# Kernel tuning notes

Measured on AMD Instinct MI355X. Metric: run time of the kernel, lower is better.

Reference implementation:

```python
import jax, jax.numpy as jnp
import numpy as np

HIDDEN = 1024
HEADS = 16
D_HEAD = HIDDEN // HEADS  # 64
N = 2048


def setup_inputs() -> dict:
    key = jax.random.key(0)
    ks = jax.random.split(key, 12)
    s = 1.0 / np.sqrt(HIDDEN)
    return {
        "q": jax.random.normal(ks[0], (N, HIDDEN), jnp.float32),
        "k": jax.random.normal(ks[1], (N, HIDDEN), jnp.float32),
        "v": jax.random.normal(ks[2], (N, HIDDEN), jnp.float32),
        "attn_bias": jax.random.normal(ks[3], (HEADS, 1, N, N), jnp.float32),
        "Wq": jax.random.normal(ks[4], (HIDDEN, HIDDEN), jnp.float32) * s,
        "bq": jax.random.normal(ks[5], (HIDDEN,), jnp.float32) * s,
        "Wk": jax.random.normal(ks[6], (HIDDEN, HIDDEN), jnp.float32) * s,
        "bk": jax.random.normal(ks[7], (HIDDEN,), jnp.float32) * s,
        "Wv": jax.random.normal(ks[8], (HIDDEN, HIDDEN), jnp.float32) * s,
        "bv": jax.random.normal(ks[9], (HIDDEN,), jnp.float32) * s,
        "Wo": jax.random.normal(ks[10], (HIDDEN, HIDDEN), jnp.float32) * s,
        "bo": jax.random.normal(ks[11], (HIDDEN,), jnp.float32) * s,
    }


def reference(q, k, v, attn_bias, Wq, bq, Wk, bk, Wv, bv, Wo, bo):
    # q,k,v: [N, hidden]; attn_bias: [H, 1, N, N]. Attention runs over the
    # node axis (dim 0 in the torch code), inner seq dim is 1 (squeezed).
    n = q.shape[0]
    scale = D_HEAD ** -0.5
    qh = (q @ Wq.T + bq).reshape(n, HEADS, D_HEAD).transpose(1, 0, 2)  # [H,N,d]
    kh = (k @ Wk.T + bk).reshape(n, HEADS, D_HEAD).transpose(1, 0, 2)  # [H,N,d]
    vh = (v @ Wv.T + bv).reshape(n, HEADS, D_HEAD).transpose(1, 0, 2)  # [H,N,d]
    scores = jnp.einsum('hnd,hmd->hnm', qh * scale, kh) + attn_bias[:, 0]  # [H,N,N]
    attn = jax.nn.softmax(scores, axis=-1)
    ctx = jnp.einsum('hnm,hmd->hnd', attn, vh)            # [H,N,d]
    ctx = ctx.transpose(1, 0, 2).reshape(n, HEADS * D_HEAD)  # [N,hidden]
    return ctx @ Wo.T + bo
```

## Files before the change

### kernel.cpp

```cpp
#include <hip/hip_runtime.h>
#include <type_traits>
#include <utility>

#define NT 2048
#define HD 1024
#define NHEAD 16
#define DHEAD 64
#define LOG2E 1.44269504f

typedef float f32x4 __attribute__((ext_vector_type(4)));
typedef __bf16 b16x8 __attribute__((ext_vector_type(8)));
typedef short s16x8 __attribute__((ext_vector_type(8)));
typedef unsigned short u16x8 __attribute__((ext_vector_type(8)));
typedef unsigned short u16x4 __attribute__((ext_vector_type(4)));

template <typename V, typename = void>
struct mfma_takes : std::false_type {};
template <typename V>
struct mfma_takes<V, std::void_t<decltype(__builtin_amdgcn_mfma_f32_16x16x32_bf16(
                         std::declval<V>(), std::declval<V>(), std::declval<f32x4>(), 0, 0, 0))>>
    : std::true_type {};

template <typename V>
__device__ __forceinline__ f32x4 mfma_impl(V a, V b, f32x4 c) {
  return __builtin_amdgcn_mfma_f32_16x16x32_bf16(a, b, c, 0, 0, 0);
}

__device__ __forceinline__ f32x4 mfma_bf16(u16x8 a, u16x8 b, f32x4 c) {
  using V = typename std::conditional<mfma_takes<b16x8>::value, b16x8, s16x8>::type;
  return mfma_impl<V>(__builtin_bit_cast(V, a), __builtin_bit_cast(V, b), c);
}

__device__ __forceinline__ unsigned short f2bf(float f) {
  unsigned int u = __builtin_bit_cast(unsigned int, f);
  return (unsigned short)((u + 0x7FFFu + ((u >> 16) & 1u)) >> 16);
}

__device__ __forceinline__ void gload16(const unsigned short* g, unsigned short* l) {
  __builtin_amdgcn_global_load_lds(
      (__attribute__((address_space(1))) void*)(void*)(g),
      (__attribute__((address_space(3))) void*)(void*)(l), 16, 0, 0);
}

__global__ __launch_bounds__(256) void cvt_bf16(
    const float* __restrict__ s0, const float* __restrict__ s1, const float* __restrict__ s2,
    const float* __restrict__ s3, const float* __restrict__ s4, const float* __restrict__ s5,
    const float* __restrict__ s6,
    unsigned short* __restrict__ d0, unsigned short* __restrict__ d1, unsigned short* __restrict__ d2,
    unsigned short* __restrict__ d3, unsigned short* __restrict__ d4, unsigned short* __restrict__ d5,
    unsigned short* __restrict__ d6) {
  const int seg = blockIdx.y;
  const float* s;
  unsigned short* d;
  switch (seg) {
    case 0: s = s0; d = d0; break;
    case 1: s = s1; d = d1; break;
    case 2: s = s2; d = d2; break;
    case 3: s = s3; d = d3; break;
    case 4: s = s4; d = d4; break;
    case 5: s = s5; d = d5; break;
    default: s = s6; d = d6; break;
  }
  const int n = (seg < 3) ? NT * HD : HD * HD;
  for (int i = blockIdx.x * 2048 + threadIdx.x * 8; i < n; i += gridDim.x * 2048) {
    f32x4 f0 = *reinterpret_cast<const f32x4*>(&s[i]);
    f32x4 f1 = *reinterpret_cast<const f32x4*>(&s[i + 4]);
    u16x8 o;
#pragma unroll
    for (int e = 0; e < 4; ++e) { o[e] = f2bf(f0[e]); o[e + 4] = f2bf(f1[e]); }
    *reinterpret_cast<u16x8*>(&d[i]) = o;
  }
}

__device__ __forceinline__ void gemm64x128(
    const unsigned short* __restrict__ A, const unsigned short* __restrict__ B,
    int n0, int m0,
    unsigned short* As0, unsigned short* As1,
    unsigned short* Bs0, unsigned short* Bs1, f32x4 acc[2][4]) {
  const int tid = threadIdx.x;
  const int lane = tid & 63;
  const int wr = (tid >> 6) >> 1, wc = (tid >> 6) & 1;
  const int srow = tid >> 3;
  const int scol = (tid & 7) << 3;

  auto stage = [&](int kt, unsigned short* as, unsigned short* bs) {
#pragma unroll
    for (int p = 0; p < 2; ++p)
      gload16(&A[(size_t)(n0 + p * 32 + srow) * HD + kt + scol], as + p * 2048 + tid * 8);
#pragma unroll
    for (int p = 0; p < 4; ++p)
      gload16(&B[(size_t)(m0 + p * 32 + srow) * HD + kt + scol], bs + p * 2048 + tid * 8);
  };
  auto comp = [&](const unsigned short* as, const unsigned short* bs) {
#pragma unroll
    for (int ks = 0; ks < 2; ++ks) {
      const int kcol = ks * 32 + (lane >> 4) * 8;
      u16x8 a[2], b[4];
#pragma unroll
      for (int i = 0; i < 2; ++i)
        a[i] = *reinterpret_cast<const u16x8*>(&as[(wr * 32 + i * 16 + (lane & 15)) * 64 + kcol]);
#pragma unroll
      for (int j = 0; j < 4; ++j)
        b[j] = *reinterpret_cast<const u16x8*>(&bs[(wc * 64 + j * 16 + (lane & 15)) * 64 + kcol]);
#pragma unroll
      for (int i = 0; i < 2; ++i)
#pragma unroll
        for (int j = 0; j < 4; ++j)
          acc[i][j] = mfma_bf16(a[i], b[j], acc[i][j]);
    }
  };

  stage(0, As0, Bs0);
  __syncthreads();
#pragma unroll 1
  for (int tt = 0; tt < 8; ++tt) {
    const int kt = tt * 128;
    stage(kt + 64, As1, Bs1);
    comp(As0, Bs0);
    __syncthreads();
    if (kt + 128 < HD) stage(kt + 128, As0, Bs0);
    comp(As1, Bs1);
    __syncthreads();
  }
}

__global__ __launch_bounds__(256) void proj_gemm(
    const unsigned short* __restrict__ qb, const unsigned short* __restrict__ kb,
    const unsigned short* __restrict__ vb,
    const unsigned short* __restrict__ Wqb, const unsigned short* __restrict__ Wkb,
    const unsigned short* __restrict__ Wvb,
    const float* __restrict__ bq, const float* __restrict__ bk, const float* __restrict__ bv,
    unsigned short* __restrict__ Qh, unsigned short* __restrict__ Kh,
    unsigned short* __restrict__ Vt) {
  const int L = blockIdx.x;
  const int m = L / 96;
  const int c = L % 96;
  const int z = c / 32;
  const int n = c % 32;
  const int n0 = n * 64, m0 = m * 128;

  const unsigned short* A = (z == 0) ? qb : (z == 1) ? kb : vb;
  const unsigned short* B = (z == 0) ? Wqb : (z == 1) ? Wkb : Wvb;
  const float* bias = (z == 0) ? bq : (z == 1) ? bk : bv;

  __shared__ unsigned short As0[64 * 64], As1[64 * 64];
  __shared__ unsigned short Bs0[128 * 64], Bs1[128 * 64];

  const int tid = threadIdx.x;
  const int lane = tid & 63;
  const int wr = (tid >> 6) >> 1, wc = (tid >> 6) & 1;

  f32x4 acc[2][4] = {};
  gemm64x128(A, B, n0, m0, As0, As1, Bs0, Bs1, acc);

  const int rgrp = (lane >> 4) * 4;
  const float scale = (z == 0) ? 0.125f * LOG2E : 1.0f;
#pragma unroll
  for (int i = 0; i < 2; ++i) {
    const int nb = n0 + wr * 32 + i * 16 + rgrp;
#pragma unroll
    for (int j = 0; j < 4; ++j) {
      const int mcol = m0 + wc * 64 + j * 16 + (lane & 15);
      const float bb = bias[mcol];
      if (z == 2) {
        u16x4 pk;
#pragma unroll
        for (int r = 0; r < 4; ++r) pk[r] = f2bf(acc[i][j][r] + bb);
        *reinterpret_cast<u16x4*>(&Vt[(size_t)mcol * NT + nb]) = pk;
      } else {
        unsigned short* dst = (z == 0) ? Qh : Kh;
#pragma unroll
        for (int r = 0; r < 4; ++r)
          dst[(size_t)(nb + r) * HD + mcol] = f2bf((acc[i][j][r] + bb) * scale);
      }
    }
  }
}

__global__ __launch_bounds__(256) void attn_kernel(
    const unsigned short* __restrict__ Qh, const unsigned short* __restrict__ Kh,
    const unsigned short* __restrict__ Vt, const float* __restrict__ bias,
    unsigned short* __restrict__ ctx) {
  const int id = blockIdx.x;
  const int xcd = id & 7, slot = id >> 3;
  const int h = xcd * 2 + (slot >> 5);
  const int q0 = (slot & 31) * 64;
  const int tid = threadIdx.x;
  const int lane = tid & 63;
  const int wave = tid >> 6;

  __shared__ unsigned short Ks[128][72];
  __shared__ unsigned short Vs[64][136];
  __shared__ unsigned short Ps[4][16][136];

  u16x8 qf[2];
  {
    const int qrow = q0 + wave * 16 + (lane & 15);
    const int db = (lane >> 4) * 8;
    qf[0] = *reinterpret_cast<const u16x8*>(&Qh[(size_t)qrow * HD + h * DHEAD + db]);
    qf[1] = *reinterpret_cast<const u16x8*>(&Qh[(size_t)qrow * HD + h * DHEAD + 32 + db]);
  }

  f32x4 oacc[4] = {};
  float mrun[4], lrun[4];
#pragma unroll
  for (int r = 0; r < 4; ++r) { mrun[r] = -3.0e38f; lrun[r] = 0.f; }

  const float* bias_h = bias + (size_t)h * NT * NT;
  const int qlrow = q0 + wave * 16 + (lane >> 4) * 4;

  const int ksr = tid >> 3, ksc = (tid & 7) << 3;
  const int vsd = tid >> 2, vsc = (tid & 3) << 3;
  const unsigned short* Kbase = Kh + h * DHEAD;
  const unsigned short* Vbase = Vt + (size_t)(h * DHEAD + vsd) * NT;

#pragma unroll
  for (int p = 0; p < 4; ++p)
    *reinterpret_cast<u16x8*>(&Ks[ksr + p * 32][ksc]) =
        *reinterpret_cast<const u16x8*>(&Kbase[(size_t)(ksr + p * 32) * HD + ksc]);
#pragma unroll
  for (int p = 0; p < 4; ++p)
    *reinterpret_cast<u16x8*>(&Vs[vsd][vsc + p * 32]) =
        *reinterpret_cast<const u16x8*>(&Vbase[vsc + p * 32]);
  __syncthreads();

  for (int t = 0; t < NT / 128; ++t) {
    const int kt = t * 128;
    float br[8][4];
    const float* bp = bias_h + (size_t)qlrow * NT + kt + (lane & 15);
#pragma unroll
    for (int j = 0; j < 8; ++j)
#pragma unroll
      for (int r = 0; r < 4; ++r) br[j][r] = bp[(size_t)r * NT + j * 16];

    u16x8 kpre[4], vpre[4];
    const bool more = (t + 1 < NT / 128);
    if (more) {
      const int kt2 = kt + 128;
#pragma unroll
      for (int p = 0; p < 4; ++p)
        kpre[p] = *reinterpret_cast<const u16x8*>(&Kbase[(size_t)(kt2 + ksr + p * 32) * HD + ksc]);
#pragma unroll
      for (int p = 0; p < 4; ++p)
        vpre[p] = *reinterpret_cast<const u16x8*>(&Vbase[kt2 + vsc + p * 32]);
    }

    f32x4 s[8] = {};
#pragma unroll
    for (int ks = 0; ks < 2; ++ks) {
      const int kcol = ks * 32 + (lane >> 4) * 8;
#pragma unroll
      for (int j = 0; j < 8; ++j) {
        u16x8 kf = *reinterpret_cast<const u16x8*>(&Ks[j * 16 + (lane & 15)][kcol]);
        s[j] = mfma_bf16(qf[ks], kf, s[j]);
      }
    }
#pragma unroll
    for (int j = 0; j < 8; ++j)
#pragma unroll
      for (int r = 0; r < 4; ++r) s[j][r] = fmaf(br[j][r], LOG2E, s[j][r]);

    float mnew[4];
#pragma unroll
    for (int r = 0; r < 4; ++r) {
      float mx = s[0][r];
#pragma unroll
      for (int j = 1; j < 8; ++j) mx = fmaxf(mx, s[j][r]);
      mx = fmaxf(mx, __shfl_xor(mx, 1));
      mx = fmaxf(mx, __shfl_xor(mx, 2));
      mx = fmaxf(mx, __shfl_xor(mx, 4));
      mx = fmaxf(mx, __shfl_xor(mx, 8));
      mnew[r] = fmaxf(mrun[r], mx);
    }
#pragma unroll
    for (int r = 0; r < 4; ++r) {
      const float corr = exp2f(mrun[r] - mnew[r]);
      lrun[r] *= corr;
#pragma unroll
      for (int nd = 0; nd < 4; ++nd) oacc[nd][r] *= corr;
      mrun[r] = mnew[r];
    }
    float psum[4] = {0.f, 0.f, 0.f, 0.f};
#pragma unroll
    for (int j = 0; j < 8; ++j)
#pragma unroll
      for (int r = 0; r < 4; ++r) {
        const float p = exp2f(s[j][r] - mrun[r]);
        psum[r] += p;
        Ps[wave][(lane >> 4) * 4 + r][j * 16 + (lane & 15)] = f2bf(p);
      }
#pragma unroll
    for (int r = 0; r < 4; ++r) {
      float tsum = psum[r];
      tsum += __shfl_xor(tsum, 1);
      tsum += __shfl_xor(tsum, 2);
      tsum += __shfl_xor(tsum, 4);
      tsum += __shfl_xor(tsum, 8);
      lrun[r] += tsum;
    }

#pragma unroll
    for (int kk = 0; kk < 4; ++kk) {
      const int kcol = kk * 32 + (lane >> 4) * 8;
      u16x8 pa = *reinterpret_cast<const u16x8*>(&Ps[wave][lane & 15][kcol]);
#pragma unroll
      for (int nd = 0; nd < 4; ++nd) {
        u16x8 vb = *reinterpret_cast<const u16x8*>(&Vs[nd * 16 + (lane & 15)][kcol]);
        oacc[nd] = mfma_bf16(pa, vb, oacc[nd]);
      }
    }
    __syncthreads();
    if (more) {
#pragma unroll
      for (int p = 0; p < 4; ++p)
        *reinterpret_cast<u16x8*>(&Ks[ksr + p * 32][ksc]) = kpre[p];
#pragma unroll
      for (int p = 0; p < 4; ++p)
        *reinterpret_cast<u16x8*>(&Vs[vsd][vsc + p * 32]) = vpre[p];
    }
    __syncthreads();
  }

#pragma unroll
  for (int nd = 0; nd < 4; ++nd) {
#pragma unroll
    for (int r = 0; r < 4; ++r) {
      const float val = oacc[nd][r] / lrun[r];
      ctx[(size_t)(qlrow + r) * HD + h * DHEAD + nd * 16 + (lane & 15)] = f2bf(val);
    }
  }
}

__global__ __launch_bounds__(256) void out_gemm(
    const unsigned short* __restrict__ Ain, const unsigned short* __restrict__ Wob,
    const float* __restrict__ bias, float* __restrict__ out) {
  const int L = blockIdx.x;
  const int m = L / 32;
  const int n = L % 32;
  const int n0 = n * 64, m0 = m * 128;

  __shared__ unsigned short As0[64 * 64], As1[64 * 64];
  __shared__ unsigned short Bs0[128 * 64], Bs1[128 * 64];

  const int tid = threadIdx.x;
  const int lane = tid & 63;
  const int wr = (tid >> 6) >> 1, wc = (tid >> 6) & 1;

  f32x4 acc[2][4] = {};
  gemm64x128(Ain, Wob, n0, m0, As0, As1, Bs0, Bs1, acc);

  const int rgrp = (lane >> 4) * 4;
#pragma unroll
  for (int i = 0; i < 2; ++i) {
    const int nb = n0 + wr * 32 + i * 16 + rgrp;
#pragma unroll
    for (int j = 0; j < 4; ++j) {
      const int mcol = m0 + wc * 64 + j * 16 + (lane & 15);
      const float bb = bias[mcol];
#pragma unroll
      for (int r = 0; r < 4; ++r)
        out[(size_t)(nb + r) * HD + mcol] = acc[i][j][r] + bb;
    }
  }
}

extern "C" void kernel_launch(void* const* d_in, const int* in_sizes, int n_in,
                              void* d_out, int out_size, void* d_ws, size_t ws_size,
                              hipStream_t stream) {
  const float* q  = (const float*)d_in[0];
  const float* k  = (const float*)d_in[1];
  const float* v  = (const float*)d_in[2];
  const float* ab = (const float*)d_in[3];
  const float* Wq = (const float*)d_in[4];
  const float* bq = (const float*)d_in[5];
  const float* Wk = (const float*)d_in[6];
  const float* bk = (const float*)d_in[7];
  const float* Wv = (const float*)d_in[8];
  const float* bv = (const float*)d_in[9];
  const float* Wo = (const float*)d_in[10];
  const float* bo = (const float*)d_in[11];

  unsigned short* qb  = (unsigned short*)d_ws;
  unsigned short* kb  = qb + (size_t)NT * HD;
  unsigned short* vb  = kb + (size_t)NT * HD;
  unsigned short* Wqb = vb + (size_t)NT * HD;
  unsigned short* Wkb = Wqb + (size_t)HD * HD;
  unsigned short* Wvb = Wkb + (size_t)HD * HD;
  unsigned short* Wob = Wvb + (size_t)HD * HD;
  unsigned short* Qh  = Wob + (size_t)HD * HD;
  unsigned short* Kh  = Qh + (size_t)NT * HD;
  unsigned short* Vt  = Kh + (size_t)NT * HD;
  unsigned short* ctx = Vt + (size_t)NT * HD;

  cvt_bf16<<<dim3(512, 7), 256, 0, stream>>>(q, k, v, Wq, Wk, Wv, Wo,
                                             qb, kb, vb, Wqb, Wkb, Wvb, Wob);
  proj_gemm<<<dim3(768), 256, 0, stream>>>(
      qb, kb, vb, Wqb, Wkb, Wvb, bq, bk, bv, Qh, Kh, Vt);
  attn_kernel<<<dim3(512), 256, 0, stream>>>(Qh, Kh, Vt, ab, ctx);
  out_gemm<<<dim3(256), 256, 0, stream>>>(ctx, Wob, bo, (float*)d_out);
}
```

Measured before the change: 132.3 us.

## Swizzle GEMM LDS tiles, deepen async staging, and prefetch attention bias

The shared GEMM helper now XOR-swizzles the LDS column chunk by row to avoid bank conflicts. It also restructures the K loop so two stages are in flight, using explicit vmcnt waits and scheduler-pinned barriers instead of __syncthreads. In the attention kernel, the bias tile for the next key block is loaded one iteration ahead and issued after the QK MFMAs so its global latency overlaps the softmax. Hand-placed waitcnt asm relies on exact load counts, so any mismatch could cause races, and keeping the bias prefetched in registers raises register pressure.

```diff
diff --git a/kernel.cpp b/kernel.cpp
--- a/kernel.cpp
+++ b/kernel.cpp
@@ -41,6 +41,15 @@
       (__attribute__((address_space(1))) void*)(void*)(g),
       (__attribute__((address_space(3))) void*)(void*)(l), 16, 0, 0);
 }
+
+__device__ __forceinline__ void barrier_pinned() {
+  __builtin_amdgcn_sched_barrier(0);
+  __builtin_amdgcn_s_barrier();
+  __builtin_amdgcn_sched_barrier(0);
+}
+#define WAIT_VM6() asm volatile("s_waitcnt vmcnt(6)" ::: "memory")
+#define WAIT_VM0() asm volatile("s_waitcnt vmcnt(0)" ::: "memory")
+#define WAIT_LGKM0() asm volatile("s_waitcnt lgkmcnt(0)" ::: "memory")
 
 __global__ __launch_bounds__(256) void cvt_bf16(
     const float* __restrict__ s0, const float* __restrict__ s1, const float* __restrict__ s2,
@@ -81,7 +90,7 @@
   const int lane = tid & 63;
   const int wr = (tid >> 6) >> 1, wc = (tid >> 6) & 1;
   const int srow = tid >> 3;
-  const int scol = (tid & 7) << 3;
+  const int scol = (((tid & 7) ^ (srow & 7)) << 3);
 
   auto stage = [&](int kt, unsigned short* as, unsigned short* bs) {
 #pragma unroll
@@ -94,14 +103,18 @@
   auto comp = [&](const unsigned short* as, const unsigned short* bs) {
 #pragma unroll
     for (int ks = 0; ks < 2; ++ks) {
-      const int kcol = ks * 32 + (lane >> 4) * 8;
+      const int q = ks * 4 + (lane >> 4);
       u16x8 a[2], b[4];
 #pragma unroll
-      for (int i = 0; i < 2; ++i)
-        a[i] = *reinterpret_cast<const u16x8*>(&as[(wr * 32 + i * 16 + (lane & 15)) * 64 + kcol]);
-#pragma unroll
-      for (int j = 0; j < 4; ++j)
-        b[j] = *reinterpret_cast<const u16x8*>(&bs[(wc * 64 + j * 16 + (lane & 15)) * 64 + kcol]);
+      for (int i = 0; i < 2; ++i) {
+        const int row = wr * 32 + i * 16 + (lane & 15);
+        a[i] = *reinterpret_cast<const u16x8*>(&as[row * 64 + ((q ^ (row & 7)) << 3)]);
+      }
+#pragma unroll
+      for (int j = 0; j < 4; ++j) {
+        const int row = wc * 64 + j * 16 + (lane & 15);
+        b[j] = *reinterpret_cast<const u16x8*>(&bs[row * 64 + ((q ^ (row & 7)) << 3)]);
+      }
 #pragma unroll
       for (int i = 0; i < 2; ++i)
 #pragma unroll
@@ -111,17 +124,22 @@
   };
 
   stage(0, As0, Bs0);
-  __syncthreads();
+  stage(64, As1, Bs1);
 #pragma unroll 1
-  for (int tt = 0; tt < 8; ++tt) {
-    const int kt = tt * 128;
-    stage(kt + 64, As1, Bs1);
-    comp(As0, Bs0);
-    __syncthreads();
-    if (kt + 128 < HD) stage(kt + 128, As0, Bs0);
-    comp(As1, Bs1);
-    __syncthreads();
-  }
+  for (int s = 0; s < 14; ++s) {
+    WAIT_VM6();
+    barrier_pinned();
+    if (s & 1) comp(As1, Bs1); else comp(As0, Bs0);
+    barrier_pinned();
+    if (s & 1) stage((s + 2) * 64, As1, Bs1);
+    else       stage((s + 2) * 64, As0, Bs0);
+  }
+  WAIT_VM6();
+  barrier_pinned();
+  comp(As0, Bs0);
+  WAIT_VM0();
+  barrier_pinned();
+  comp(As1, Bs1);
 }
 
 __global__ __launch_bounds__(256) void proj_gemm(
@@ -214,6 +232,14 @@
   const unsigned short* Kbase = Kh + h * DHEAD;
   const unsigned short* Vbase = Vt + (size_t)(h * DHEAD + vsd) * NT;
 
+  float br[8][4];
+  {
+    const float* bp = bias_h + (size_t)qlrow * NT + (lane & 15);
+#pragma unroll
+    for (int j = 0; j < 8; ++j)
+#pragma unroll
+      for (int r = 0; r < 4; ++r) br[j][r] = bp[(size_t)r * NT + j * 16];
+  }
 #pragma unroll
   for (int p = 0; p < 4; ++p)
     *reinterpret_cast<u16x8*>(&Ks[ksr + p * 32][ksc]) =
@@ -222,29 +248,11 @@
   for (int p = 0; p < 4; ++p)
     *reinterpret_cast<u16x8*>(&Vs[vsd][vsc + p * 32]) =
         *reinterpret_cast<const u16x8*>(&Vbase[vsc + p * 32]);
-  __syncthreads();
-
+  WAIT_LGKM0();
+  barrier_pinned();
+
+#pragma unroll 1
   for (int t = 0; t < NT / 128; ++t) {
-    const int kt = t * 128;
-    float br[8][4];
-    const float* bp = bias_h + (size_t)qlrow * NT + kt + (lane & 15);
-#pragma unroll
-    for (int j = 0; j < 8; ++j)
-#pragma unroll
-      for (int r = 0; r < 4; ++r) br[j][r] = bp[(size_t)r * NT + j * 16];
-
-    u16x8 kpre[4], vpre[4];
-    const bool more = (t + 1 < NT / 128);
-    if (more) {
-      const int kt2 = kt + 128;
-#pragma unroll
-      for (int p = 0; p < 4; ++p)
-        kpre[p] = *reinterpret_cast<const u16x8*>(&Kbase[(size_t)(kt2 + ksr + p * 32) * HD + ksc]);
-#pragma unroll
-      for (int p = 0; p < 4; ++p)
-        vpre[p] = *reinterpret_cast<const u16x8*>(&Vbase[kt2 + vsc + p * 32]);
-    }
-
     f32x4 s[8] = {};
 #pragma unroll
     for (int ks = 0; ks < 2; ++ks) {
@@ -259,6 +267,23 @@
     for (int j = 0; j < 8; ++j)
 #pragma unroll
       for (int r = 0; r < 4; ++r) s[j][r] = fmaf(br[j][r], LOG2E, s[j][r]);
+
+    const bool more = (t + 1 < NT / 128);
+    u16x8 kpre[4], vpre[4];
+    if (more) {
+      const int kt2 = (t + 1) * 128;
+      const float* bp = bias_h + (size_t)qlrow * NT + kt2 + (lane & 15);
+#pragma unroll
+      for (int j = 0; j < 8; ++j)
+#pragma unroll
+        for (int r = 0; r < 4; ++r) br[j][r] = bp[(size_t)r * NT + j * 16];
+#pragma unroll
+      for (int p = 0; p < 4; ++p)
+        kpre[p] = *reinterpret_cast<const u16x8*>(&Kbase[(size_t)(kt2 + ksr + p * 32) * HD + ksc]);
+#pragma unroll
+      for (int p = 0; p < 4; ++p)
+        vpre[p] = *reinterpret_cast<const u16x8*>(&Vbase[kt2 + vsc + p * 32]);
+    }
 
     float mnew[4];
 #pragma unroll
@@ -309,7 +334,8 @@
         oacc[nd] = mfma_bf16(pa, vb, oacc[nd]);
       }
     }
-    __syncthreads();
+
+    barrier_pinned();
     if (more) {
 #pragma unroll
       for (int p = 0; p < 4; ++p)
@@ -318,7 +344,8 @@
       for (int p = 0; p < 4; ++p)
         *reinterpret_cast<u16x8*>(&Vs[vsd][vsc + p * 32]) = vpre[p];
     }
-    __syncthreads();
+    WAIT_LGKM0();
+    barrier_pinned();
   }
 
 #pragma unroll
```

Result: faster. 124.5 us (-5.9%).
